# Kernel optimization log

Hardware: AMD Instinct MI355X
Metric: run time of the kernel (lower is better)

Reference implementation:

```python
import jax, jax.numpy as jnp
import numpy as np
import math

D_MODEL = 4096
NUM_HEADS = 32
NUM_KV_HEADS = 8
HEAD_DIM = D_MODEL // NUM_HEADS  # 128
GROUP = NUM_HEADS // NUM_KV_HEADS  # 4
SEQ_LEN = 2048
BATCH = 2
ROPE_THETA = 10000.0


def apply_rope(x, start_pos=0):
    # x: [b, h, s, hd]; llama-style rotation on interleaved (even, odd) pairs
    b, h, s, hd = x.shape
    inv_freq = 1.0 / (ROPE_THETA ** (jnp.arange(0, hd, 2, dtype=jnp.float32) / hd))  # [hd/2]
    pos = jnp.arange(start_pos, start_pos + s, dtype=jnp.float32)  # [s]
    ang = pos[:, None] * inv_freq[None, :]  # [s, hd/2]
    cos = jnp.cos(ang).astype(x.dtype)
    sin = jnp.sin(ang).astype(x.dtype)
    xr = x[..., 0::2]  # [b,h,s,hd/2]
    xi = x[..., 1::2]
    out_r = xr * cos - xi * sin
    out_i = xr * sin + xi * cos
    return jnp.stack([out_r, out_i], axis=-1).reshape(b, h, s, hd)


def setup_inputs() -> dict:
    key = jax.random.key(0)
    ks = jax.random.split(key, 5)
    qkv_dim = HEAD_DIM * (NUM_HEADS + 2 * NUM_KV_HEADS)  # 6144
    scale = 1.0 / math.sqrt(D_MODEL)
    return {
        "x": jax.random.normal(ks[0], (BATCH, SEQ_LEN, D_MODEL), jnp.float32),
        "w_qkv": jax.random.normal(ks[1], (qkv_dim, D_MODEL), jnp.float32) * scale,
        "b_qkv": jax.random.normal(ks[2], (qkv_dim,), jnp.float32) * 0.01,
        "w_o": jax.random.normal(ks[3], (D_MODEL, D_MODEL), jnp.float32) * scale,
        "b_o": jax.random.normal(ks[4], (D_MODEL,), jnp.float32) * 0.01,
    }


def reference(x, w_qkv, b_qkv, w_o, b_o):
    bs, seq_len, d_model = x.shape
    qkv = x @ w_qkv.T + b_qkv  # [b, s, 6144]
    q_dim = NUM_HEADS * HEAD_DIM
    kv_dim = NUM_KV_HEADS * HEAD_DIM
    q, k, v = jnp.split(qkv, [q_dim, q_dim + kv_dim], axis=-1)
    q = q.reshape(bs, seq_len, NUM_HEADS, HEAD_DIM).transpose(0, 2, 1, 3)
    k = k.reshape(bs, seq_len, NUM_KV_HEADS, HEAD_DIM).transpose(0, 2, 1, 3)
    v = v.reshape(bs, seq_len, NUM_KV_HEADS, HEAD_DIM).transpose(0, 2, 1, 3)
    q = apply_rope(q, 0)
    k = apply_rope(k, 0)
    # repeat_kv: kv head i -> q heads [i*group, (i+1)*group)
    k = jnp.repeat(k, GROUP, axis=1)  # [b, H, s, hd]
    v = jnp.repeat(v, GROUP, axis=1)
    scores = jnp.einsum("bhqd,bhkd->bhqk", q, k) / math.sqrt(HEAD_DIM)
    causal = jnp.tril(jnp.ones((seq_len, seq_len), dtype=bool))
    scores = jnp.where(causal[None, None, :, :], scores, jnp.float32(-1e20))
    attn = jax.nn.softmax(scores, axis=-1)
    out = jnp.einsum("bhqk,bhkd->bhqd", attn, v)
    out = out.transpose(0, 2, 1, 3).reshape(bs, seq_len, d_model)
    return out @ w_o.T + b_o
```

## Files before the change

kernel.cpp:

```cpp
#include <hip/hip_runtime.h>

typedef unsigned short u16;
typedef unsigned int   u32;

#define BATCH   2
#define SEQ     2048
#define DMODEL  4096
#define NHEADS  32
#define NKV     8
#define HDIM    128
#define QKV_DIM 6144

typedef __bf16 bf16x8 __attribute__((ext_vector_type(8)));
typedef float  f32x4  __attribute__((ext_vector_type(4)));

__device__ __forceinline__ float b2f(u16 u) {
  u32 x = ((u32)u) << 16;
  return __builtin_bit_cast(float, x);
}
__device__ __forceinline__ u16 f2b(float f) {
  u32 x = __builtin_bit_cast(u32, f);
  x = (x + 0x7FFFu + ((x >> 16) & 1u)) >> 16;
  return (u16)x;
}
__device__ __forceinline__ float b2f_lo(u32 p) { return __builtin_bit_cast(float, p << 16); }
__device__ __forceinline__ float b2f_hi(u32 p) { return __builtin_bit_cast(float, p & 0xFFFF0000u); }

__device__ __forceinline__ u32 pk(float a, float b) {
  return (u32)f2b(a) | ((u32)f2b(b) << 16);
}

__device__ __forceinline__ void gload16(const u16* __restrict__ g, u16* l) {
  __builtin_amdgcn_global_load_lds(
      (const __attribute__((address_space(1))) unsigned int*)(const void*)g,
      (__attribute__((address_space(3))) unsigned int*)(void*)l,
      16, 0, 0);
}

__global__ __launch_bounds__(256) void f32_to_bf16(const float* __restrict__ in,
                                                   u16* __restrict__ out, int n8) {
  const int i = blockIdx.x * 256 + threadIdx.x;
  if (i >= n8) return;
  const float4* p = (const float4*)(in + (size_t)i * 8);
  const float4 a = p[0], b = p[1];
  uint4 r;
  r.x = pk(a.x, a.y); r.y = pk(a.z, a.w); r.z = pk(b.x, b.y); r.w = pk(b.z, b.w);
  ((uint4*)out)[i] = r;
}

template <int MODE>
__global__ __launch_bounds__(256) void gemm_bt2(const u16* __restrict__ Ab,
                                                const u16* __restrict__ Bw,
                                                const float* __restrict__ bias,
                                                float* __restrict__ outf,
                                                u16* __restrict__ oq,
                                                u16* __restrict__ ok,
                                                u16* __restrict__ ov,
                                                int K, int N) {
  __shared__ u16 As[128 * 64];
  __shared__ u16 Bs[128 * 64];
  const int t    = threadIdx.x;
  const int lane = t & 63;
  const int wv   = t >> 6;
  const int wr   = wv >> 1, wc = wv & 1;
  const int q4   = lane >> 4, l15 = lane & 15;

  const int nwgx = gridDim.x;
  const int nwg  = nwgx * gridDim.y;
  int bid = blockIdx.y * nwgx + blockIdx.x;
  const int cpx = nwg >> 3;
  bid = (bid & 7) * cpx + (bid >> 3);
  const int m0 = (bid / nwgx) * 128, n0 = (bid % nwgx) * 128;

  f32x4 acc[4][4] = {};

  for (int k0 = 0; k0 < K; k0 += 64) {
    __syncthreads();
#pragma unroll
    for (int i = 0; i < 4; i++) {
      const int u = t + i * 256;
      const int r = u >> 3, c8 = (u & 7) * 8;
      gload16(Bw + (size_t)(n0 + r) * K + k0 + c8, &Bs[u * 8]);
    }
#pragma unroll
    for (int i = 0; i < 4; i++) {
      const int u = t + i * 256;
      const int r = u >> 3, c8 = (u & 7) * 8;
      gload16(Ab + (size_t)(m0 + r) * K + k0 + c8, &As[u * 8]);
    }
    __syncthreads();

#pragma unroll
    for (int kk = 0; kk < 2; kk++) {
      bf16x8 af[4], bfr[4];
#pragma unroll
      for (int i = 0; i < 4; i++)
        af[i] = *(const bf16x8*)&As[(wr * 64 + i * 16 + l15) * 64 + kk * 32 + q4 * 8];
#pragma unroll
      for (int j = 0; j < 4; j++)
        bfr[j] = *(const bf16x8*)&Bs[(wc * 64 + j * 16 + l15) * 64 + kk * 32 + q4 * 8];
#pragma unroll
      for (int i = 0; i < 4; i++)
#pragma unroll
        for (int j = 0; j < 4; j++)
          acc[i][j] = __builtin_amdgcn_mfma_f32_16x16x32_bf16(af[i], bfr[j], acc[i][j], 0, 0, 0);
    }
  }

  const int col = l15, quad = q4;
#pragma unroll
  for (int j = 0; j < 4; j++) {
    const int gn = n0 + wc * 64 + j * 16 + col;
    const float bv = bias[gn];
#pragma unroll
    for (int i = 0; i < 4; i++) {
      const int gmb = m0 + wr * 64 + i * 16 + quad * 4;
#pragma unroll
      for (int rr = 0; rr < 4; rr++) {
        float val = acc[i][j][rr] + bv;
        const int gm = gmb + rr;
        if (MODE == 1) {
          outf[(size_t)gm * N + gn] = val;
        } else {
          const int b = gm >> 11, s = gm & (SEQ - 1);
          const int d = gn & (HDIM - 1);
          if (gn < 4096) {
            val *= 0.08838834764831845f;
            const int hh = gn >> 7;
            oq[((size_t)(b * NHEADS + hh) * SEQ + s) * HDIM + d] = f2b(val);
          } else if (gn < 5120) {
            const int hh = (gn - 4096) >> 7;
            ok[((size_t)(b * NKV + hh) * SEQ + s) * HDIM + d] = f2b(val);
          } else {
            const int hh = (gn - 5120) >> 7;
            ov[((size_t)(b * NKV + hh) * SEQ + s) * HDIM + d] = f2b(val);
          }
        }
      }
    }
  }
}

__global__ __launch_bounds__(256) void rope_kernel(u16* __restrict__ q, u16* __restrict__ kk,
                                                   int qrows, int totrows) {
  const int idx = blockIdx.x * 256 + threadIdx.x;
  const int row = idx >> 6;
  const int i   = idx & 63;
  if (row >= totrows) return;
  u16* base;
  int r;
  if (row < qrows) { base = q  + (size_t)row * HDIM;           r = row; }
  else             { base = kk + (size_t)(row - qrows) * HDIM; r = row - qrows; }
  const int s = r & (SEQ - 1);
  const float l2theta = 13.287712379549449f;
  const float inv = exp2f(-((float)(2 * i) * (1.0f / 128.0f)) * l2theta);
  const float ang = (float)s * inv;
  const float c  = cosf(ang);
  const float sn = sinf(ang);
  const u32 xv = *(const u32*)&base[2 * i];
  const float xr = b2f_lo(xv), xi = b2f_hi(xv);
  *(u32*)&base[2 * i] = pk(xr * c - xi * sn, xr * sn + xi * c);
}

__global__ __launch_bounds__(256, 2) void attn_mfma(const u16* __restrict__ q,
                                                    const u16* __restrict__ k,
                                                    const u16* __restrict__ v,
                                                    u16* __restrict__ out) {
  __shared__ u16 Ks[64 * 136];
  __shared__ u16 VtBuf[128 * 72];
  __shared__ u32 Ps32[4 * 32 * 36];
  u32* Vt32 = (u32*)VtBuf;

  const int t    = threadIdx.x;
  const int lane = t & 63;
  const int w    = t >> 6;
  const int q4   = lane >> 4, l15 = lane & 15;
  const int qb   = 15 - (int)blockIdx.x;
  const int h = blockIdx.y, b = blockIdx.z;
  const int m0 = qb * 128;
  const int mw = m0 + w * 32;
  const int kvh = h >> 2;
  const u16* Qp = q + (size_t)(b * NHEADS + h) * SEQ * HDIM;
  const u16* Kp = k + (size_t)(b * NKV + kvh) * SEQ * HDIM;
  const u16* Vp = v + (size_t)(b * NKV + kvh) * SEQ * HDIM;

  bf16x8 qf[2][4];
#pragma unroll
  for (int rt = 0; rt < 2; rt++)
#pragma unroll
    for (int kk = 0; kk < 4; kk++)
      qf[rt][kk] = *(const bf16x8*)&Qp[(size_t)(mw + rt * 16 + l15) * HDIM + kk * 32 + q4 * 8];

  f32x4 oacc[2][8] = {};
  float mrow[2], lrow[2];
  mrow[0] = mrow[1] = -1e30f;
  lrow[0] = lrow[1] = 0.f;

  u32* Pw32 = &Ps32[w * 32 * 36];

  const int nch = qb * 2 + 2;
  for (int kc = 0; kc < nch; kc++) {
#pragma unroll
    for (int i = 0; i < 4; i++) {
      const int u = t + i * 256;
      const int r = u >> 4, c = (u & 15) * 8;
      *(uint4*)&Ks[r * 136 + c] = *(const uint4*)&Kp[(size_t)(kc * 64 + r) * HDIM + c];
    }
    uint2 e0[4], e1[4];
#pragma unroll
    for (int i = 0; i < 4; i++) {
      const int tau = t + i * 256;
      const int k2 = tau >> 5, dq = tau & 31;
      e0[i] = *(const uint2*)&Vp[(size_t)(kc * 64 + 2 * k2) * HDIM + dq * 4];
      e1[i] = *(const uint2*)&Vp[(size_t)(kc * 64 + 2 * k2 + 1) * HDIM + dq * 4];
    }
    __syncthreads();

    const bool part = (kc * 64 <= mw + 31);
    if (part) {
      const bool fullch = (kc * 64 + 63 <= mw);
      f32x4 sacc[2][4] = {};
      __builtin_amdgcn_s_setprio(1);
#pragma unroll
      for (int ct = 0; ct < 4; ct++) {
#pragma unroll
        for (int kk = 0; kk < 4; kk++) {
          const bf16x8 kb = *(const bf16x8*)&Ks[(ct * 16 + l15) * 136 + kk * 32 + q4 * 8];
          sacc[0][ct] = __builtin_amdgcn_mfma_f32_16x16x32_bf16(kb, qf[0][kk], sacc[0][ct], 0, 0, 0);
          sacc[1][ct] = __builtin_amdgcn_mfma_f32_16x16x32_bf16(kb, qf[1][kk], sacc[1][ct], 0, 0, 0);
        }
      }
      __builtin_amdgcn_s_setprio(0);
#pragma unroll
      for (int rt = 0; rt < 2; rt++) {
        float p[4][4];
        float cm[4];
        const int mm = mw + rt * 16 + l15;
#pragma unroll
        for (int ct = 0; ct < 4; ct++) {
#pragma unroll
          for (int rr = 0; rr < 4; rr++) {
            float s = sacc[rt][ct][rr];
            if (!fullch) {
              const int key = kc * 64 + ct * 16 + q4 * 4 + rr;
              s = (key <= mm) ? s : -1e30f;
            }
            p[ct][rr] = s;
          }
          cm[ct] = fmaxf(fmaxf(p[ct][0], p[ct][1]), fmaxf(p[ct][2], p[ct][3]));
        }
        float vmax = fmaxf(fmaxf(cm[0], cm[1]), fmaxf(cm[2], cm[3]));
        vmax = fmaxf(vmax, __shfl_xor(vmax, 16));
        vmax = fmaxf(vmax, __shfl_xor(vmax, 32));
        const float nm = fmaxf(mrow[rt], vmax);
        const float alpha = __expf(mrow[rt] - nm);
        mrow[rt] = nm;
        float cs[4];
#pragma unroll
        for (int ct = 0; ct < 4; ct++) {
#pragma unroll
          for (int rr = 0; rr < 4; rr++) p[ct][rr] = __expf(p[ct][rr] - nm);
          cs[ct] = (p[ct][0] + p[ct][1]) + (p[ct][2] + p[ct][3]);
        }
        lrow[rt] = lrow[rt] * alpha + ((cs[0] + cs[1]) + (cs[2] + cs[3]));
#pragma unroll
        for (int ct = 0; ct < 4; ct++) {
          uint2 w2;
          w2.x = pk(p[ct][0], p[ct][1]);
          w2.y = pk(p[ct][2], p[ct][3]);
          *(uint2*)&Pw32[(rt * 16 + l15) * 36 + ct * 8 + q4 * 2] = w2;
        }
        float alT[4];
#pragma unroll
        for (int rr = 0; rr < 4; rr++) alT[rr] = __shfl(alpha, q4 * 4 + rr, 64);
#pragma unroll
        for (int dt = 0; dt < 8; dt++)
#pragma unroll
          for (int rr = 0; rr < 4; rr++) oacc[rt][dt][rr] *= alT[rr];
      }
    }
#pragma unroll
    for (int i = 0; i < 4; i++) {
      const int tau = t + i * 256;
      const int k2 = tau >> 5, dq = tau & 31;
      u32 wj[4];
      wj[0] = (e0[i].x & 0xFFFFu) | (e1[i].x << 16);
      wj[1] = (e0[i].x >> 16)     | (e1[i].x & 0xFFFF0000u);
      wj[2] = (e0[i].y & 0xFFFFu) | (e1[i].y << 16);
      wj[3] = (e0[i].y >> 16)     | (e1[i].y & 0xFFFF0000u);
      const int g = k2 >> 2;
#pragma unroll
      for (int j = 0; j < 4; j++) {
        const int d = dq * 4 + j;
        const int gs = g ^ ((d >> 3) & 7);
        Vt32[d * 36 + gs * 4 + (k2 & 3)] = wj[j];
      }
    }
    __syncthreads();

    if (part) {
      __builtin_amdgcn_s_setprio(1);
#pragma unroll
      for (int kk2 = 0; kk2 < 2; kk2++) {
        bf16x8 pa[2];
        pa[0] = *(const bf16x8*)&Pw32[(l15) * 36 + kk2 * 16 + q4 * 4];
        pa[1] = *(const bf16x8*)&Pw32[(16 + l15) * 36 + kk2 * 16 + q4 * 4];
#pragma unroll
        for (int dt = 0; dt < 8; dt++) {
          const int d = dt * 16 + l15;
          const int gs = (kk2 * 4 + q4) ^ ((d >> 3) & 7);
          const bf16x8 vb = *(const bf16x8*)&Vt32[d * 36 + gs * 4];
          oacc[0][dt] = __builtin_amdgcn_mfma_f32_16x16x32_bf16(pa[0], vb, oacc[0][dt], 0, 0, 0);
          oacc[1][dt] = __builtin_amdgcn_mfma_f32_16x16x32_bf16(pa[1], vb, oacc[1][dt], 0, 0, 0);
        }
      }
      __builtin_amdgcn_s_setprio(0);
    }
  }

#pragma unroll
  for (int rt = 0; rt < 2; rt++) {
    float ls = lrow[rt];
    ls += __shfl_xor(ls, 16);
    ls += __shfl_xor(ls, 32);
#pragma unroll
    for (int rr = 0; rr < 4; rr++) {
      const float lt = __shfl(ls, q4 * 4 + rr, 64);
      const float inv = 1.0f / lt;
      const int mm = mw + rt * 16 + q4 * 4 + rr;
      u16* op = &out[((size_t)(b * SEQ + mm)) * DMODEL + h * HDIM + l15];
#pragma unroll
      for (int dt = 0; dt < 8; dt++)
        op[dt * 16] = f2b(oacc[rt][dt][rr] * inv);
    }
  }
}

extern "C" void kernel_launch(void* const* d_in, const int* in_sizes, int n_in,
                              void* d_out, int out_size, void* d_ws, size_t ws_size,
                              hipStream_t stream) {
  const float* x     = (const float*)d_in[0];
  const float* w_qkv = (const float*)d_in[1];
  const float* b_qkv = (const float*)d_in[2];
  const float* w_o   = (const float*)d_in[3];
  const float* b_o   = (const float*)d_in[4];
  float* out = (float*)d_out;

  const size_t QN = (size_t)BATCH * NHEADS * SEQ * HDIM;
  const size_t KN = (size_t)BATCH * NKV * SEQ * HDIM;

  u16* q    = (u16*)d_ws;
  u16* k    = q + QN;
  u16* v    = k + KN;
  u16* attn = v + KN;
  u16* wb   = attn + QN;
  u16* xb   = attn;

  const dim3 blk(256);

  const int n8_x = BATCH * SEQ * DMODEL / 8;
  f32_to_bf16<<<dim3(n8_x / 256), blk, 0, stream>>>(x, xb, n8_x);
  const int n8_qkv = QKV_DIM * DMODEL / 8;
  f32_to_bf16<<<dim3(n8_qkv / 256), blk, 0, stream>>>(w_qkv, wb, n8_qkv);

  gemm_bt2<0><<<dim3(QKV_DIM / 128, (BATCH * SEQ) / 128), blk, 0, stream>>>(
      xb, wb, b_qkv, nullptr, q, k, v, DMODEL, QKV_DIM);

  const int qrows = BATCH * NHEADS * SEQ;
  const int totrows = qrows + BATCH * NKV * SEQ;
  rope_kernel<<<dim3((totrows * 64) / 256), blk, 0, stream>>>(q, k, qrows, totrows);

  attn_mfma<<<dim3(SEQ / 128, NHEADS, BATCH), blk, 0, stream>>>(q, k, v, attn);

  const int n8_o = DMODEL * DMODEL / 8;
  f32_to_bf16<<<dim3(n8_o / 256), blk, 0, stream>>>(w_o, wb, n8_o);

  gemm_bt2<1><<<dim3(DMODEL / 128, (BATCH * SEQ) / 128), blk, 0, stream>>>(
      attn, wb, b_o, out, nullptr, nullptr, nullptr, DMODEL, DMODEL);
}
```

Measured before the change: 997.9 us.

## Use 256x256 GEMM tiles with 512 threads and double-buffered LDS staging

```diff
diff --git a/kernel.cpp b/kernel.cpp
--- a/kernel.cpp
+++ b/kernel.cpp
@@ -49,7 +49,7 @@
 }
 
 template <int MODE>
-__global__ __launch_bounds__(256) void gemm_bt2(const u16* __restrict__ Ab,
+__global__ __launch_bounds__(512) void gemm_bt3(const u16* __restrict__ Ab,
                                                 const u16* __restrict__ Bw,
                                                 const float* __restrict__ bias,
                                                 float* __restrict__ outf,
@@ -57,12 +57,12 @@
                                                 u16* __restrict__ ok,
                                                 u16* __restrict__ ov,
                                                 int K, int N) {
-  __shared__ u16 As[128 * 64];
-  __shared__ u16 Bs[128 * 64];
+  __shared__ u16 As[2][256 * 64];
+  __shared__ u16 Bs[2][256 * 64];
   const int t    = threadIdx.x;
   const int lane = t & 63;
   const int wv   = t >> 6;
-  const int wr   = wv >> 1, wc = wv & 1;
+  const int wr   = wv >> 2, wc = wv & 3;
   const int q4   = lane >> 4, l15 = lane & 15;
 
   const int nwgx = gridDim.x;
@@ -70,51 +70,62 @@
   int bid = blockIdx.y * nwgx + blockIdx.x;
   const int cpx = nwg >> 3;
   bid = (bid & 7) * cpx + (bid >> 3);
-  const int m0 = (bid / nwgx) * 128, n0 = (bid % nwgx) * 128;
-
-  f32x4 acc[4][4] = {};
-
-  for (int k0 = 0; k0 < K; k0 += 64) {
-    __syncthreads();
-#pragma unroll
-    for (int i = 0; i < 4; i++) {
-      const int u = t + i * 256;
+  const int m0 = (bid / nwgx) * 256, n0 = (bid % nwgx) * 256;
+
+  f32x4 acc[8][4] = {};
+
+  auto STAGE = [&](int buf, int k0) {
+#pragma unroll
+    for (int i = 0; i < 4; i++) {
+      const int u = t + i * 512;
       const int r = u >> 3, c8 = (u & 7) * 8;
-      gload16(Bw + (size_t)(n0 + r) * K + k0 + c8, &Bs[u * 8]);
-    }
-#pragma unroll
-    for (int i = 0; i < 4; i++) {
-      const int u = t + i * 256;
+      gload16(Bw + (size_t)(n0 + r) * K + k0 + c8, &Bs[buf][u * 8]);
+    }
+#pragma unroll
+    for (int i = 0; i < 4; i++) {
+      const int u = t + i * 512;
       const int r = u >> 3, c8 = (u & 7) * 8;
-      gload16(Ab + (size_t)(m0 + r) * K + k0 + c8, &As[u * 8]);
-    }
-    __syncthreads();
-
+      gload16(Ab + (size_t)(m0 + r) * K + k0 + c8, &As[buf][u * 8]);
+    }
+  };
+
+  auto COMPUTE = [&](int buf) {
 #pragma unroll
     for (int kk = 0; kk < 2; kk++) {
-      bf16x8 af[4], bfr[4];
-#pragma unroll
-      for (int i = 0; i < 4; i++)
-        af[i] = *(const bf16x8*)&As[(wr * 64 + i * 16 + l15) * 64 + kk * 32 + q4 * 8];
+      bf16x8 af[8], bfr[4];
+#pragma unroll
+      for (int i = 0; i < 8; i++)
+        af[i] = *(const bf16x8*)&As[buf][(wr * 128 + i * 16 + l15) * 64 + kk * 32 + q4 * 8];
 #pragma unroll
       for (int j = 0; j < 4; j++)
-        bfr[j] = *(const bf16x8*)&Bs[(wc * 64 + j * 16 + l15) * 64 + kk * 32 + q4 * 8];
-#pragma unroll
-      for (int i = 0; i < 4; i++)
+        bfr[j] = *(const bf16x8*)&Bs[buf][(wc * 64 + j * 16 + l15) * 64 + kk * 32 + q4 * 8];
+#pragma unroll
+      for (int i = 0; i < 8; i++)
 #pragma unroll
         for (int j = 0; j < 4; j++)
           acc[i][j] = __builtin_amdgcn_mfma_f32_16x16x32_bf16(af[i], bfr[j], acc[i][j], 0, 0, 0);
     }
+  };
+
+  STAGE(0, 0);
+  __syncthreads();
+
+  int cur = 0;
+  for (int k0 = 64; k0 < K; k0 += 64) {
+    STAGE(cur ^ 1, k0);
+    COMPUTE(cur);
+    __syncthreads();
+    cur ^= 1;
   }
-
-  const int col = l15, quad = q4;
+  COMPUTE(cur);
+
 #pragma unroll
   for (int j = 0; j < 4; j++) {
-    const int gn = n0 + wc * 64 + j * 16 + col;
+    const int gn = n0 + wc * 64 + j * 16 + l15;
     const float bv = bias[gn];
 #pragma unroll
-    for (int i = 0; i < 4; i++) {
-      const int gmb = m0 + wr * 64 + i * 16 + quad * 4;
+    for (int i = 0; i < 8; i++) {
+      const int gmb = m0 + wr * 128 + i * 16 + q4 * 4;
 #pragma unroll
       for (int rr = 0; rr < 4; rr++) {
         float val = acc[i][j][rr] + bv;
@@ -357,13 +368,14 @@
   u16* xb   = attn;
 
   const dim3 blk(256);
+  const dim3 blk512(512);
 
   const int n8_x = BATCH * SEQ * DMODEL / 8;
   f32_to_bf16<<<dim3(n8_x / 256), blk, 0, stream>>>(x, xb, n8_x);
   const int n8_qkv = QKV_DIM * DMODEL / 8;
   f32_to_bf16<<<dim3(n8_qkv / 256), blk, 0, stream>>>(w_qkv, wb, n8_qkv);
 
-  gemm_bt2<0><<<dim3(QKV_DIM / 128, (BATCH * SEQ) / 128), blk, 0, stream>>>(
+  gemm_bt3<0><<<dim3(QKV_DIM / 256, (BATCH * SEQ) / 256), blk512, 0, stream>>>(
       xb, wb, b_qkv, nullptr, q, k, v, DMODEL, QKV_DIM);
 
   const int qrows = BATCH * NHEADS * SEQ;
@@ -375,6 +387,6 @@
   const int n8_o = DMODEL * DMODEL / 8;
   f32_to_bf16<<<dim3(n8_o / 256), blk, 0, stream>>>(w_o, wb, n8_o);
 
-  gemm_bt2<1><<<dim3(DMODEL / 128, (BATCH * SEQ) / 128), blk, 0, stream>>>(
+  gemm_bt3<1><<<dim3(DMODEL / 256, (BATCH * SEQ) / 256), blk512, 0, stream>>>(
       attn, wb, b_o, out, nullptr, nullptr, nullptr, DMODEL, DMODEL);
 }
```

New measurement: 1.037 ms. 1.04x slower.
